# Performance work log

Hardware: AMD Instinct MI355X
Metric: run time of the kernel (lower is better)

Reference implementation:

```python
import jax, jax.numpy as jnp
import numpy as np

K = 16
EPS = 1e-5
NEG_SLOPE = 0.2


def leaky(x):
    return jnp.where(x > 0, x, NEG_SLOPE * x)


def batchnorm_train(x, gamma, beta):
    # x: [B, D]; training-mode BN with biased variance (torch semantics)
    mean = jnp.mean(x, axis=0)
    var = jnp.mean((x - mean) ** 2, axis=0)
    return (x - mean) * jax.lax.rsqrt(var + EPS) * gamma + beta


def setup_inputs() -> dict:
    key = jax.random.key(0)
    ks = jax.random.split(key, 20)
    N, M, D = 30000, 8000, 16
    s = lambda fan_in: 1.0 / np.sqrt(fan_in)
    inp = {
        "xyz": jax.random.normal(ks[0], (N, 3), jnp.float32),
        "atom_xyz": jax.random.normal(ks[1], (M, 3), jnp.float32),
        "atom_types": jax.random.normal(ks[2], (M, D), jnp.float32),
        "Wt1": jax.random.uniform(ks[3], (D, D), jnp.float32, -s(D), s(D)),
        "bt1": jax.random.uniform(ks[4], (D,), jnp.float32, -s(D), s(D)),
        "Wt2": jax.random.uniform(ks[5], (D, D), jnp.float32, -s(D), s(D)),
        "bt2": jax.random.uniform(ks[6], (D,), jnp.float32, -s(D), s(D)),
        "Wt3": jax.random.uniform(ks[7], (D, D), jnp.float32, -s(D), s(D)),
        "bt3": jax.random.uniform(ks[8], (D,), jnp.float32, -s(D), s(D)),
        # embed: conv1 Linear(D+1, D), conv2 Linear(D, D), conv3 Linear(2D, D)
        "W1": jax.random.uniform(ks[9], (D + 1, D), jnp.float32, -s(D + 1), s(D + 1)),
        "b1": jax.random.uniform(ks[10], (D,), jnp.float32, -s(D + 1), s(D + 1)),
        "W2": jax.random.uniform(ks[11], (D, D), jnp.float32, -s(D), s(D)),
        "b2": jax.random.uniform(ks[12], (D,), jnp.float32, -s(D), s(D)),
        "W3": jax.random.uniform(ks[13], (2 * D, D), jnp.float32, -s(2 * D), s(2 * D)),
        "b3": jax.random.uniform(ks[14], (D,), jnp.float32, -s(2 * D), s(2 * D)),
        # batchnorm affine params
        "g1": jnp.ones((D,), jnp.float32),
        "be1": jnp.zeros((D,), jnp.float32),
        "g2": jnp.ones((D,), jnp.float32),
        "be2": jnp.zeros((D,), jnp.float32),
    }
    return inp


def reference(xyz, atom_xyz, atom_types,
              Wt1, bt1, Wt2, bt2, Wt3, bt3,
              W1, b1, W2, b2, W3, b3, g1, be1, g2, be2):
    N, D = xyz.shape[0], atom_types.shape[1]

    # transform_types MLP on atom features: [M, D]
    t = leaky(atom_types @ Wt1 + bt1)
    t = leaky(t @ Wt2 + bt2)
    t = leaky(t @ Wt3 + bt3)

    # kNN: squared distances via GEMM expansion (avoids [N,M,3])
    d2 = (jnp.sum(xyz ** 2, axis=1, keepdims=True)
          + jnp.sum(atom_xyz ** 2, axis=1)[None, :]
          - 2.0 * xyz @ atom_xyz.T)                      # [N, M]
    _, idx = jax.lax.top_k(-d2, K)                       # [N, K] nearest atoms

    # gather neighbor coords, recompute exact squared dists (as in source)
    y_ik = atom_xyz[idx]                                 # [N, K, 3]
    dists = jnp.sum((xyz[:, None, :] - y_ik) ** 2, axis=-1)  # [N, K]

    feat = jnp.concatenate([t[idx], (1.0 / dists)[..., None]], axis=-1)  # [N,K,D+1]

    # conv1 -> leaky -> bn1 -> sum-pool
    fx = feat @ W1 + b1                                  # [N, K, D]
    fx = batchnorm_train(leaky(fx).reshape(-1, D), g1, be1).reshape(N, K, D)
    fx1 = fx.sum(axis=1)                                 # [N, D]

    # conv2 -> leaky -> bn2 -> sum-pool
    fx = fx @ W2 + b2
    fx = batchnorm_train(leaky(fx).reshape(-1, D), g2, be2).reshape(N, K, D)
    fx2 = fx.sum(axis=1)                                 # [N, D]

    return jnp.concatenate([fx1, fx2], axis=-1) @ W3 + b3  # [N, D]
```

## Files before the change

### kernel.cpp

```cpp
#include <hip/hip_runtime.h>

#define N_PTS   30000
#define M_ATOMS 8000
#define D       16
#define KNN     16
#define NGRP    125
#define EPS     1e-5f
#define SLOPE   0.2f
#define BN_COUNT 480000.0f

typedef unsigned long long ull;

__device__ __forceinline__ float leaky(float x) { return x > 0.f ? x : SLOPE * x; }

__device__ __forceinline__ unsigned fkey(float f) {
  unsigned u = __float_as_uint(f);
  return u ^ ((u & 0x80000000u) ? 0xFFFFFFFFu : 0x80000000u);
}
__device__ __forceinline__ float unfkey(unsigned e) {
  unsigned u = (e & 0x80000000u) ? (e ^ 0x80000000u) : ~e;
  return __uint_as_float(u);
}

#define DPPSTEP32(v, CTRL) {                                                   \
  unsigned t_ = (unsigned)__builtin_amdgcn_update_dpp(-1, (int)(v), CTRL, 0xF, 0xF, false); \
  (v) = t_ < (v) ? t_ : (v); }

__device__ __forceinline__ unsigned wmin32d(unsigned v) {
  DPPSTEP32(v, 0x111); DPPSTEP32(v, 0x112); DPPSTEP32(v, 0x114);
  DPPSTEP32(v, 0x118); DPPSTEP32(v, 0x142); DPPSTEP32(v, 0x143);
  return (unsigned)__builtin_amdgcn_readlane((int)v, 63);
}

__device__ __forceinline__ void cswap(ull& a, ull& b) {
  ull mn = a < b ? a : b, mx = a < b ? b : a;
  a = mn; b = mx;
}

__device__ __forceinline__ int morton_cell(float x, float y, float z) {
  int cx = min(max((int)floorf((x + 4.f) * 2.f), 0), 15);
  int cy = min(max((int)floorf((y + 4.f) * 2.f), 0), 15);
  int cz = min(max((int)floorf((z + 4.f) * 2.f), 0), 15);
  int c = 0;
#pragma unroll
  for (int b = 0; b < 4; ++b)
    c |= (((cx>>b)&1) << (3*b)) | (((cy>>b)&1) << (3*b+1)) | (((cz>>b)&1) << (3*b+2));
  return c;
}

__global__ void __launch_bounds__(1024) kB_hist_scan(
    const float* __restrict__ atom_xyz, int* __restrict__ cursors,
    float* __restrict__ gstats, unsigned* __restrict__ benc) {
  __shared__ int h0[4096], h1[4096];
  int tid = threadIdx.x;
  for (int i = tid; i < 4096; i += 1024) h0[i] = 0;
  if (tid < 288) gstats[tid] = 0.f;
  if (tid >= 288 && tid < 663) benc[tid - 288] = 0xFFFFFFFFu;
  if (tid >= 663 && tid < 1024) benc[tid - 288] = 0u;
  if (tid < 14) benc[736 + tid] = 0u;
  __syncthreads();
  for (int m = tid; m < M_ATOMS; m += 1024) {
    int c = morton_cell(atom_xyz[m*3], atom_xyz[m*3+1], atom_xyz[m*3+2]);
    atomicAdd(&h0[c], 1);
  }
  __syncthreads();
  int* src = h0; int* dst = h1;
  for (int off = 1; off < 4096; off <<= 1) {
    for (int i = tid; i < 4096; i += 1024) {
      int v = src[i];
      if (i >= off) v += src[i-off];
      dst[i] = v;
    }
    __syncthreads();
    int* t = src; src = dst; dst = t;
  }
  for (int i = tid; i < 4096; i += 1024) cursors[i] = i ? src[i-1] : 0;
}

#define LAYER(IN, OUT, W, B)                                        \
  _Pragma("unroll") for (int j = 0; j < 16; ++j) {                  \
    float acc = B[j];                                               \
    _Pragma("unroll") for (int i = 0; i < 16; ++i)                  \
      acc = fmaf(IN[i], W[i*16+j], acc);                            \
    OUT[j] = leaky(acc);                                            \
  }

__global__ void __launch_bounds__(256) kC_scatter_mlp(
    const float* __restrict__ atom_xyz, const float* __restrict__ atom_types,
    const float* __restrict__ Wt1, const float* __restrict__ bt1,
    const float* __restrict__ Wt2, const float* __restrict__ bt2,
    const float* __restrict__ Wt3, const float* __restrict__ bt3,
    const float* __restrict__ W1, const float* __restrict__ b1,
    int* __restrict__ cursors, float4* __restrict__ atoms4s,
    int* __restrict__ origid, unsigned* __restrict__ benc,
    float* __restrict__ tu_out) {
  __shared__ float w1[256], w2[256], w3[256], wc[256];
  __shared__ float bb1[16], bb2[16], bb3[16], bbc[16];
  int tid = threadIdx.x;
  w1[tid] = Wt1[tid]; w2[tid] = Wt2[tid]; w3[tid] = Wt3[tid]; wc[tid] = W1[tid];
  if (tid < 16) { bb1[tid] = bt1[tid]; bb2[tid] = bt2[tid];
                  bb3[tid] = bt3[tid]; bbc[tid] = b1[tid]; }
  __syncthreads();
  int m = blockIdx.x * 256 + tid;
  if (m >= M_ATOMS) return;

  float x = atom_xyz[m*3], y = atom_xyz[m*3+1], z = atom_xyz[m*3+2];
  int c = morton_cell(x, y, z);
  int pos = atomicAdd(&cursors[c], 1);
  atoms4s[pos] = make_float4(x, y, z, fmaf(x,x, fmaf(y,y, z*z)));
  origid[pos] = m;
  int g = pos >> 6;
  atomicMin(&benc[g],       fkey(x)); atomicMax(&benc[375+g], fkey(x));
  atomicMin(&benc[125+g],   fkey(y)); atomicMax(&benc[500+g], fkey(y));
  atomicMin(&benc[250+g],   fkey(z)); atomicMax(&benc[625+g], fkey(z));

  float u[16], v[16];
  const float4* tp = (const float4*)(atom_types + (size_t)m*16);
  float4 q0 = tp[0], q1 = tp[1], q2 = tp[2], q3 = tp[3];
  u[0]=q0.x; u[1]=q0.y; u[2]=q0.z; u[3]=q0.w;
  u[4]=q1.x; u[5]=q1.y; u[6]=q1.z; u[7]=q1.w;
  u[8]=q2.x; u[9]=q2.y; u[10]=q2.z; u[11]=q2.w;
  u[12]=q3.x; u[13]=q3.y; u[14]=q3.z; u[15]=q3.w;
  LAYER(u, v, w1, bb1);
  LAYER(v, u, w2, bb2);
  LAYER(u, v, w3, bb3);
  float up[16];
#pragma unroll
  for (int j = 0; j < 16; ++j) {
    float acc = bbc[j];
#pragma unroll
    for (int i = 0; i < 16; ++i) acc = fmaf(v[i], wc[i*16+j], acc);
    up[j] = acc;
  }
  float4* op = (float4*)(tu_out + (size_t)m*16);
  op[0] = make_float4(up[0], up[1], up[2], up[3]);
  op[1] = make_float4(up[4], up[5], up[6], up[7]);
  op[2] = make_float4(up[8], up[9], up[10], up[11]);
  op[3] = make_float4(up[12], up[13], up[14], up[15]);
}

__global__ void __launch_bounds__(256) k2_knn(
    const float* __restrict__ xyz, const float4* __restrict__ atoms4s,
    const int* __restrict__ origid, const unsigned* __restrict__ benc,
    const float* __restrict__ atom_xyz, const float* __restrict__ tu,
    const float* __restrict__ W1,
    int2* __restrict__ pairs, float* __restrict__ gstats) {
  __shared__ float sbuf[4*16*20];
  int tid = threadIdx.x;
  int lane = tid & 63;
  int wid = tid >> 6;
  int n = blockIdx.x * 4 + wid;

  float px = xyz[n*3+0], py = xyz[n*3+1], pz = xyz[n*3+2];
  float x2 = fmaf(px,px, fmaf(py,py, pz*pz));

  unsigned ea, eb = 0xFFFFFFFFu;
  {
    int g = lane;
    float mnx = unfkey(benc[g]),     mny = unfkey(benc[125+g]), mnz = unfkey(benc[250+g]);
    float mxx = unfkey(benc[375+g]), mxy = unfkey(benc[500+g]), mxz = unfkey(benc[625+g]);
    float dx = fmaxf(fmaxf(mnx - px, px - mxx), 0.f);
    float dy = fmaxf(fmaxf(mny - py, py - mxy), 0.f);
    float dz = fmaxf(fmaxf(mnz - pz, pz - mxz), 0.f);
    float lb = fmaf(dx,dx, fmaf(dy,dy, dz*dz)) * 0.999f - 1e-4f;
    ea = (fkey(lb) & 0xFFFFFF00u) | (unsigned)g;
  }
  if (lane + 64 < NGRP) {
    int g = lane + 64;
    float mnx = unfkey(benc[g]),     mny = unfkey(benc[125+g]), mnz = unfkey(benc[250+g]);
    float mxx = unfkey(benc[375+g]), mxy = unfkey(benc[500+g]), mxz = unfkey(benc[625+g]);
    float dx = fmaxf(fmaxf(mnx - px, px - mxx), 0.f);
    float dy = fmaxf(fmaxf(mny - py, py - mxy), 0.f);
    float dz = fmaxf(fmaxf(mnz - pz, pz - mxz), 0.f);
    float lb = fmaf(dx,dx, fmaf(dy,dy, dz*dz)) * 0.999f - 1e-4f;
    eb = (fkey(lb) & 0xFFFFFF00u) | (unsigned)g;
  }
  unsigned cur = ea < eb ? ea : eb;
  unsigned bak = ea < eb ? eb : ea;

  int gs[4];
#pragma unroll
  for (int r = 0; r < 4; ++r) {
    unsigned m = wmin32d(cur);
    bool own = (cur == m);
    cur = own ? bak : cur;
    bak = own ? 0xFFFFFFFFu : bak;
    gs[r] = (int)(m & 0xFFu);
  }

  float4 A[4]; int OI[4];
#pragma unroll
  for (int r = 0; r < 4; ++r) {
    int base = gs[r] << 6;
    A[r]  = atoms4s[base + lane];
    OI[r] = origid [base + lane];
  }
  ull E[4];
#pragma unroll
  for (int r = 0; r < 4; ++r) {
    float dotp = fmaf(px,A[r].x, fmaf(py,A[r].y, pz*A[r].z));
    float d2 = (x2 + A[r].w) - 2.f*dotp;
    E[r] = ((ull)fkey(d2) << 32) | (unsigned)OI[r];
  }
  cswap(E[0],E[1]); cswap(E[2],E[3]); cswap(E[0],E[2]);
  cswap(E[1],E[3]); cswap(E[1],E[2]);
  unsigned cf0 = (unsigned)(E[0] >> 32), ci0 = (unsigned)E[0];
  unsigned cf1 = (unsigned)(E[1] >> 32), ci1 = (unsigned)E[1];
  unsigned cf2 = (unsigned)(E[2] >> 32), ci2 = (unsigned)E[2];
  unsigned cf3 = (unsigned)(E[3] >> 32), ci3 = (unsigned)E[3];

  ull res = ~0ull;
  unsigned mf = 0, mi = 0;
  for (int r = 0; r < KNN; ++r) {
    mf = wmin32d(cf0);
    ull ball = __ballot(cf0 == mf);
    if (__popcll(ball) == 1) {
      int srcl = (int)(__ffsll(ball) - 1);
      mi = (unsigned)__builtin_amdgcn_readlane((int)ci0, srcl);
    } else {
      unsigned cand = (cf0 == mf) ? ci0 : 0xFFFFFFFFu;
      mi = wmin32d(cand);
    }
    bool own = (cf0 == mf) && (ci0 == mi);
    if (lane == r) res = (((ull)mf) << 32) | mi;
    cf0 = own ? cf1 : cf0; cf1 = own ? cf2 : cf1;
    cf2 = own ? cf3 : cf2; cf3 = own ? 0xFFFFFFFFu : cf3;
    ci0 = own ? ci1 : ci0; ci1 = own ? ci2 : ci1;
    ci2 = own ? ci3 : ci2; ci3 = own ? 0xFFFFFFFFu : ci3;
  }
  ull lv = res;
  ull thresh = (((ull)mf) << 32) | mi;

  for (int it = 0; it < NGRP - 4; ++it) {
    unsigned m = wmin32d(cur);
    if ((m & 0xFFFFFF00u) >= (unsigned)(thresh >> 32)) break;
    bool own = (cur == m);
    cur = own ? bak : cur;
    bak = own ? 0xFFFFFFFFu : bak;
    int base = (int)(m & 0xFFu) << 6;

    float4 a = atoms4s[base + lane];
    int oi2 = origid[base + lane];
    float dotp = fmaf(px,a.x, fmaf(py,a.y, pz*a.z));
    float d2 = (x2 + a.w) - 2.f*dotp;
    ull key = ((ull)fkey(d2) << 32) | (unsigned)oi2;

    ull mk = __ballot(key < thresh);
    while (mk) {
      int src = (int)(__ffsll(mk) - 1);
      mk &= mk - 1;
      unsigned klo = (unsigned)__builtin_amdgcn_readlane((int)(unsigned)key, src);
      unsigned khi = (unsigned)__builtin_amdgcn_readlane((int)(unsigned)(key >> 32), src);
      ull kc = ((ull)khi << 32) | klo;
      if (kc < thresh) {
        bool ins = (lane < KNN) && (kc < lv);
        unsigned pvlo = (unsigned)__builtin_amdgcn_update_dpp(0, (int)(unsigned)lv,        0x111, 0xF, 0xF, false);
        unsigned pvhi = (unsigned)__builtin_amdgcn_update_dpp(0, (int)(unsigned)(lv>>32), 0x111, 0xF, 0xF, false);
        int pins      =           __builtin_amdgcn_update_dpp(0, ins ? 1 : 0,              0x111, 0xF, 0xF, false);
        if (ins) lv = pins ? (((ull)pvhi << 32) | pvlo) : kc;
        unsigned tlo = (unsigned)__builtin_amdgcn_readlane((int)(unsigned)lv, KNN-1);
        unsigned thi = (unsigned)__builtin_amdgcn_readlane((int)(unsigned)(lv >> 32), KNN-1);
        thresh = ((ull)thi << 32) | tlo;
      }
    }
  }

  int oi = (int)(unsigned)(lv & 0xFFFFFFFFull);
  float iv = 0.f;
  if (lane < KNN) {
    float bx = atom_xyz[oi*3+0], by = atom_xyz[oi*3+1], bz = atom_xyz[oi*3+2];
    float dx = px - bx, dy = py - by, dz = pz - bz;
    float dd = fmaf(dx,dx, fmaf(dy,dy, dz*dz));
    iv = 1.f / dd;
    pairs[n*KNN + lane] = make_int2(oi, __float_as_int(iv));

    const float4* up4 = (const float4*)(tu + (size_t)oi*16);
    float4 u0 = up4[0], u1 = up4[1], u2 = up4[2], u3 = up4[3];
    float4* row = (float4*)&sbuf[(wid*16 + lane)*20];
    float4 w;
    w.x = leaky(fmaf(iv, W1[256+ 0], u0.x)); w.y = leaky(fmaf(iv, W1[256+ 1], u0.y));
    w.z = leaky(fmaf(iv, W1[256+ 2], u0.z)); w.w = leaky(fmaf(iv, W1[256+ 3], u0.w));
    row[0] = w;
    w.x = leaky(fmaf(iv, W1[256+ 4], u1.x)); w.y = leaky(fmaf(iv, W1[256+ 5], u1.y));
    w.z = leaky(fmaf(iv, W1[256+ 6], u1.z)); w.w = leaky(fmaf(iv, W1[256+ 7], u1.w));
    row[1] = w;
    w.x = leaky(fmaf(iv, W1[256+ 8], u2.x)); w.y = leaky(fmaf(iv, W1[256+ 9], u2.y));
    w.z = leaky(fmaf(iv, W1[256+10], u2.z)); w.w = leaky(fmaf(iv, W1[256+11], u2.w));
    row[2] = w;
    w.x = leaky(fmaf(iv, W1[256+12], u3.x)); w.y = leaky(fmaf(iv, W1[256+13], u3.y));
    w.z = leaky(fmaf(iv, W1[256+14], u3.z)); w.w = leaky(fmaf(iv, W1[256+15], u3.w));
    row[3] = w;
  }
  __syncthreads();
  {
    int ch = tid & 15, grp = tid >> 4;
    float S = 0.f, Q = 0.f;
#pragma unroll
    for (int i = 0; i < 4; ++i) {
      float v = sbuf[(grp*4 + i)*20 + ch];
      S += v; Q += v*v;
    }
    __syncthreads();
    sbuf[grp*20 + ch] = S;
    sbuf[400 + grp*20 + ch] = Q;
  }
  __syncthreads();
  if (tid < 32) {
    int ch = tid & 15;
    int off = (tid < 16) ? 0 : 400;
    float s = 0.f;
#pragma unroll
    for (int g = 0; g < 16; ++g) s += sbuf[off + g*20 + ch];
    atomicAdd(&gstats[(blockIdx.x & 7)*32 + tid], s);
  }
}

__device__ __forceinline__ void a1_row(const float* __restrict__ tu, int idx,
                                       float iv, const float* wiv, float* a) {
  const float4* up = (const float4*)(tu + (size_t)idx*16);
  float4 r0 = up[0], r1 = up[1], r2 = up[2], r3 = up[3];
  float u[16];
  u[0]=r0.x; u[1]=r0.y; u[2]=r0.z; u[3]=r0.w;
  u[4]=r1.x; u[5]=r1.y; u[6]=r1.z; u[7]=r1.w;
  u[8]=r2.x; u[9]=r2.y; u[10]=r2.z; u[11]=r2.w;
  u[12]=r3.x; u[13]=r3.y; u[14]=r3.z; u[15]=r3.w;
#pragma unroll
  for (int j = 0; j < 16; ++j) a[j] = leaky(fmaf(iv, wiv[j], u[j]));
}

__global__ void __launch_bounds__(256, 4) k4_main(
    const int2* __restrict__ pairs, const float* __restrict__ tu,
    const float* __restrict__ W1,
    const float* __restrict__ W2, const float* __restrict__ b2,
    const float* __restrict__ g1, const float* __restrict__ be1,
    float* __restrict__ fx1_out, float* __restrict__ s2_out,
    float* __restrict__ gstats) {
  __shared__ float wiv[16], w2s[256], b2s[16];
  __shared__ float sc1[16], sh1[16];
  __shared__ float buf[16*16*17];
  int tid = threadIdx.x;
  w2s[tid] = W2[tid];
  if (tid < 16) { wiv[tid] = W1[256 + tid]; b2s[tid] = b2[tid]; }
  if (tid < 16) {
    float s1 = 0.f, q1 = 0.f;
#pragma unroll
    for (int c = 0; c < 8; ++c) { s1 += gstats[c*32 + tid]; q1 += gstats[c*32 + 16 + tid]; }
    float mean = s1 * (1.f/BN_COUNT);
    float var  = q1 * (1.f/BN_COUNT) - mean*mean;
    float sC = g1[tid] / sqrtf(var + EPS);
    sc1[tid] = sC;
    sh1[tid] = be1[tid] - mean * sC;
  }
  __syncthreads();

  int g = blockIdx.x * 256 + tid;
  int p = tid >> 4, k = tid & 15;
  int2 pr = pairs[g];
  int idx = pr.x;
  float iv = __int_as_float(pr.y);
  float h[16], a2[16];
  a1_row(tu, idx, iv, wiv, h);
#pragma unroll
  for (int j = 0; j < 16; ++j) h[j] = fmaf(h[j], sc1[j], sh1[j]);
#pragma unroll
  for (int j = 0; j < 16; ++j) {
    float accj = b2s[j];
#pragma unroll
    for (int i = 0; i < 16; ++i) accj = fmaf(h[i], w2s[i*16+j], accj);
    a2[j] = leaky(accj);
  }

  float* myrow = &buf[(p*16 + k)*17];
  int p2 = tid >> 4, j2 = tid & 15;
#pragma unroll
  for (int j = 0; j < 16; ++j) myrow[j] = h[j];
  __syncthreads();
  {
    float s = 0.f;
#pragma unroll
    for (int kk = 0; kk < 16; ++kk) s += buf[(p2*16+kk)*17 + j2];
    fx1_out[(size_t)blockIdx.x*256 + tid] = s;
  }
  __syncthreads();
#pragma unroll
  for (int j = 0; j < 16; ++j) myrow[j] = a2[j];
  __syncthreads();
  float s2v = 0.f;
#pragma unroll
  for (int kk = 0; kk < 16; ++kk) s2v += buf[(p2*16+kk)*17 + j2];
  s2_out[(size_t)blockIdx.x*256 + tid] = s2v;
  __syncthreads();
#pragma unroll
  for (int j = 0; j < 16; ++j) myrow[j] = a2[j]*a2[j];
  __syncthreads();
  float q2v = 0.f;
#pragma unroll
  for (int kk = 0; kk < 16; ++kk) q2v += buf[(p2*16+kk)*17 + j2];
  __syncthreads();
  buf[p2*17 + j2] = s2v;
  buf[289 + p2*17 + j2] = q2v;
  __syncthreads();
  if (tid < 16) {
    float t1 = 0.f, t2 = 0.f;
#pragma unroll
    for (int pp = 0; pp < 16; ++pp) { t1 += buf[pp*17 + tid]; t2 += buf[289 + pp*17 + tid]; }
    atomicAdd(&gstats[256 + tid], t1);
    atomicAdd(&gstats[272 + tid], t2);
  }
}

__global__ void __launch_bounds__(256) k5_final(
    const float* __restrict__ fx1_in, const float* __restrict__ s2_in,
    const float* __restrict__ gstats,
    const float* __restrict__ W3, const float* __restrict__ b3,
    const float* __restrict__ g2, const float* __restrict__ be2,
    float* __restrict__ out) {
  __shared__ float w[512], bb[16], sc2[16], sh2[16];
  int tid = threadIdx.x;
  w[tid] = W3[tid]; w[256+tid] = W3[256+tid];
  if (tid < 16) {
    bb[tid] = b3[tid];
    float mean = gstats[256+tid] * (1.f/BN_COUNT);
    float var  = gstats[272+tid] * (1.f/BN_COUNT) - mean*mean;
    float s = g2[tid] / sqrtf(var + EPS);
    sc2[tid] = s;
    sh2[tid] = be2[tid] - mean * s;
  }
  __syncthreads();
  int n = blockIdx.x * 256 + tid;
  if (n >= N_PTS) return;

  const float4* f1p = (const float4*)(fx1_in + (size_t)n*16);
  const float4* f2p = (const float4*)(s2_in  + (size_t)n*16);
  float4 x0=f1p[0], x1=f1p[1], x2=f1p[2], x3=f1p[3];
  float4 y0=f2p[0], y1=f2p[1], y2=f2p[2], y3=f2p[3];
  float f1[16] = {x0.x,x0.y,x0.z,x0.w, x1.x,x1.y,x1.z,x1.w,
                  x2.x,x2.y,x2.z,x2.w, x3.x,x3.y,x3.z,x3.w};
  float f2[16] = {y0.x,y0.y,y0.z,y0.w, y1.x,y1.y,y1.z,y1.w,
                  y2.x,y2.y,y2.z,y2.w, y3.x,y3.y,y3.z,y3.w};
#pragma unroll
  for (int i = 0; i < 16; ++i) f2[i] = fmaf(sc2[i], f2[i], 16.f * sh2[i]);

  float4* op = (float4*)(out + (size_t)n*16);
  float o[16];
#pragma unroll
  for (int j = 0; j < 16; ++j) {
    float accj = bb[j];
#pragma unroll
    for (int i = 0; i < 16; ++i) accj = fmaf(f1[i], w[i*16+j], accj);
#pragma unroll
    for (int i = 0; i < 16; ++i) accj = fmaf(f2[i], w[(16+i)*16+j], accj);
    o[j] = accj;
  }
  op[0] = make_float4(o[0], o[1], o[2], o[3]);
  op[1] = make_float4(o[4], o[5], o[6], o[7]);
  op[2] = make_float4(o[8], o[9], o[10], o[11]);
  op[3] = make_float4(o[12], o[13], o[14], o[15]);
}

extern "C" void kernel_launch(void* const* d_in, const int* in_sizes, int n_in,
                              void* d_out, int out_size, void* d_ws, size_t ws_size,
                              hipStream_t stream) {
  const float* xyz        = (const float*)d_in[0];
  const float* atom_xyz   = (const float*)d_in[1];
  const float* atom_types = (const float*)d_in[2];
  const float* Wt1 = (const float*)d_in[3];  const float* bt1 = (const float*)d_in[4];
  const float* Wt2 = (const float*)d_in[5];  const float* bt2 = (const float*)d_in[6];
  const float* Wt3 = (const float*)d_in[7];  const float* bt3 = (const float*)d_in[8];
  const float* W1  = (const float*)d_in[9];  const float* b1  = (const float*)d_in[10];
  const float* W2  = (const float*)d_in[11]; const float* b2  = (const float*)d_in[12];
  const float* W3  = (const float*)d_in[13]; const float* b3  = (const float*)d_in[14];
  const float* g1  = (const float*)d_in[15]; const float* be1 = (const float*)d_in[16];
  const float* g2  = (const float*)d_in[17]; const float* be2 = (const float*)d_in[18];
  float* out = (float*)d_out;

  float* ws = (float*)d_ws;
  float*    tu      = ws;
  int2*     pairs   = (int2*)(ws + 128000);
  float*    fx1     = ws + 1088000;
  float*    s2      = ws + 1568000;
  float*    gstats  = ws + 2048000;
  int*      cursors = (int*)(ws + 2048288);
  unsigned* benc    = (unsigned*)(ws + 2052384);
  float4*   atoms4s = (float4*)(ws + 1088000);
  int*      origid  = (int*)(ws + 1120000);

  kB_hist_scan<<<1, 1024, 0, stream>>>(atom_xyz, cursors, gstats, benc);
  kC_scatter_mlp<<<32, 256, 0, stream>>>(atom_xyz, atom_types, Wt1, bt1,
                                         Wt2, bt2, Wt3, bt3, W1, b1,
                                         cursors, atoms4s, origid, benc, tu);
  k2_knn<<<7500, 256, 0, stream>>>(xyz, atoms4s, origid, benc, atom_xyz,
                                   tu, W1, pairs, gstats);
  k4_main<<<1875, 256, 0, stream>>>(pairs, tu, W1, W2, b2, g1, be1,
                                    fx1, s2, gstats);
  k5_final<<<118, 256, 0, stream>>>(fx1, s2, gstats, W3, b3, g2, be2, out);
}
```

Baseline: 215.5 us.

## Replace sorted kNN seeding with radix-select threshold and unsorted candidate set

The initial top-16 is now chosen by a bitwise radix select over the 256 candidate keys using ballot/popcount, instead of 16 rounds of wavefront min extraction. Survivors are compacted through shared memory into an unsorted 16-lane list. During later insertion, the current maximum is replaced and a DPP 64-bit max reduction recomputes the threshold, instead of shifting a sorted list. This removes serial min-extraction rounds, but each radix select costs 32 iterations of 4 ballots, and each insertion now pays a full 64-bit max reduction.

```diff
diff --git a/kernel.cpp b/kernel.cpp
--- a/kernel.cpp
+++ b/kernel.cpp
@@ -32,9 +32,20 @@
   return (unsigned)__builtin_amdgcn_readlane((int)v, 63);
 }
 
-__device__ __forceinline__ void cswap(ull& a, ull& b) {
-  ull mn = a < b ? a : b, mx = a < b ? b : a;
-  a = mn; b = mx;
+#define DPPSTEP64MAX(lo, hi, CTRL) {                                           \
+  unsigned tlo_ = (unsigned)__builtin_amdgcn_update_dpp(0, (int)(lo), CTRL, 0xF, 0xF, false); \
+  unsigned thi_ = (unsigned)__builtin_amdgcn_update_dpp(0, (int)(hi), CTRL, 0xF, 0xF, false); \
+  bool gt_ = (thi_ > (hi)) || ((thi_ == (hi)) && (tlo_ > (lo)));               \
+  (lo) = gt_ ? tlo_ : (lo); (hi) = gt_ ? thi_ : (hi); }
+
+__device__ __forceinline__ ull wmax64d(ull v) {
+  unsigned lo = (unsigned)v, hi = (unsigned)(v >> 32);
+  DPPSTEP64MAX(lo, hi, 0x111); DPPSTEP64MAX(lo, hi, 0x112);
+  DPPSTEP64MAX(lo, hi, 0x114); DPPSTEP64MAX(lo, hi, 0x118);
+  DPPSTEP64MAX(lo, hi, 0x142); DPPSTEP64MAX(lo, hi, 0x143);
+  unsigned flo = (unsigned)__builtin_amdgcn_readlane((int)lo, 63);
+  unsigned fhi = (unsigned)__builtin_amdgcn_readlane((int)hi, 63);
+  return ((ull)fhi << 32) | flo;
 }
 
 __device__ __forceinline__ int morton_cell(float x, float y, float z) {
@@ -145,7 +156,7 @@
     const float* __restrict__ atom_xyz, const float* __restrict__ tu,
     const float* __restrict__ W1,
     int2* __restrict__ pairs, float* __restrict__ gstats) {
-  __shared__ float sbuf[4*16*20];
+  __shared__ float sbuf[4*16*20 + 128];
   int tid = threadIdx.x;
   int lane = tid & 63;
   int wid = tid >> 6;
@@ -195,41 +206,69 @@
     A[r]  = atoms4s[base + lane];
     OI[r] = origid [base + lane];
   }
-  ull E[4];
-#pragma unroll
-  for (int r = 0; r < 4; ++r) {
-    float dotp = fmaf(px,A[r].x, fmaf(py,A[r].y, pz*A[r].z));
-    float d2 = (x2 + A[r].w) - 2.f*dotp;
-    E[r] = ((ull)fkey(d2) << 32) | (unsigned)OI[r];
-  }
-  cswap(E[0],E[1]); cswap(E[2],E[3]); cswap(E[0],E[2]);
-  cswap(E[1],E[3]); cswap(E[1],E[2]);
-  unsigned cf0 = (unsigned)(E[0] >> 32), ci0 = (unsigned)E[0];
-  unsigned cf1 = (unsigned)(E[1] >> 32), ci1 = (unsigned)E[1];
-  unsigned cf2 = (unsigned)(E[2] >> 32), ci2 = (unsigned)E[2];
-  unsigned cf3 = (unsigned)(E[3] >> 32), ci3 = (unsigned)E[3];
-
-  ull res = ~0ull;
-  unsigned mf = 0, mi = 0;
-  for (int r = 0; r < KNN; ++r) {
-    mf = wmin32d(cf0);
-    ull ball = __ballot(cf0 == mf);
-    if (__popcll(ball) == 1) {
-      int srcl = (int)(__ffsll(ball) - 1);
-      mi = (unsigned)__builtin_amdgcn_readlane((int)ci0, srcl);
-    } else {
-      unsigned cand = (cf0 == mf) ? ci0 : 0xFFFFFFFFu;
-      mi = wmin32d(cand);
+  unsigned cf0, cf1, cf2, cf3, ci0, ci1, ci2, ci3;
+  {
+    float d0 = (x2 + A[0].w) - 2.f*fmaf(px,A[0].x, fmaf(py,A[0].y, pz*A[0].z));
+    float d1 = (x2 + A[1].w) - 2.f*fmaf(px,A[1].x, fmaf(py,A[1].y, pz*A[1].z));
+    float d2 = (x2 + A[2].w) - 2.f*fmaf(px,A[2].x, fmaf(py,A[2].y, pz*A[2].z));
+    float d3 = (x2 + A[3].w) - 2.f*fmaf(px,A[3].x, fmaf(py,A[3].y, pz*A[3].z));
+    cf0 = fkey(d0); cf1 = fkey(d1); cf2 = fkey(d2); cf3 = fkey(d3);
+    ci0 = (unsigned)OI[0]; ci1 = (unsigned)OI[1];
+    ci2 = (unsigned)OI[2]; ci3 = (unsigned)OI[3];
+  }
+
+  unsigned F = 0;
+  for (int b = 31; b >= 0; --b) {
+    unsigned x = F | (1u << b);
+    int c = __popcll(__ballot(cf0 < x)) + __popcll(__ballot(cf1 < x))
+          + __popcll(__ballot(cf2 < x)) + __popcll(__ballot(cf3 < x));
+    if (c < KNN) F = x;
+  }
+  ull m0 = __ballot(cf0 == F), m1 = __ballot(cf1 == F);
+  ull m2 = __ballot(cf2 == F), m3 = __ballot(cf3 == F);
+  int c_eq = __popcll(m0) + __popcll(m1) + __popcll(m2) + __popcll(m3);
+  unsigned I;
+  if (c_eq == 1) {
+    if (m0)      I = (unsigned)__builtin_amdgcn_readlane((int)ci0, (int)(__ffsll(m0)-1));
+    else if (m1) I = (unsigned)__builtin_amdgcn_readlane((int)ci1, (int)(__ffsll(m1)-1));
+    else if (m2) I = (unsigned)__builtin_amdgcn_readlane((int)ci2, (int)(__ffsll(m2)-1));
+    else         I = (unsigned)__builtin_amdgcn_readlane((int)ci3, (int)(__ffsll(m3)-1));
+  } else {
+    int c_lt = __popcll(__ballot(cf0 < F)) + __popcll(__ballot(cf1 < F))
+             + __popcll(__ballot(cf2 < F)) + __popcll(__ballot(cf3 < F));
+    int j = KNN - c_lt;
+    unsigned P = 0;
+    for (int b = 31; b >= 0; --b) {
+      unsigned x = P | (1u << b);
+      int c = __popcll(__ballot(cf0 == F && ci0 < x))
+            + __popcll(__ballot(cf1 == F && ci1 < x))
+            + __popcll(__ballot(cf2 == F && ci2 < x))
+            + __popcll(__ballot(cf3 == F && ci3 < x));
+      if (c < j) P = x;
     }
-    bool own = (cf0 == mf) && (ci0 == mi);
-    if (lane == r) res = (((ull)mf) << 32) | mi;
-    cf0 = own ? cf1 : cf0; cf1 = own ? cf2 : cf1;
-    cf2 = own ? cf3 : cf2; cf3 = own ? 0xFFFFFFFFu : cf3;
-    ci0 = own ? ci1 : ci0; ci1 = own ? ci2 : ci1;
-    ci2 = own ? ci3 : ci2; ci3 = own ? 0xFFFFFFFFu : ci3;
-  }
-  ull lv = res;
-  ull thresh = (((ull)mf) << 32) | mi;
+    I = P;
+  }
+  ull T = ((ull)F << 32) | I;
+
+  {
+    unsigned* scr = (unsigned*)&sbuf[4*16*20 + wid*32];
+    ull E0 = ((ull)cf0 << 32) | ci0, E1 = ((ull)cf1 << 32) | ci1;
+    ull E2 = ((ull)cf2 << 32) | ci2, E3 = ((ull)cf3 << 32) | ci3;
+    bool s0 = E0 <= T, s1 = E1 <= T, s2 = E2 <= T, s3 = E3 <= T;
+    ull b0 = __ballot(s0), b1 = __ballot(s1), b2 = __ballot(s2), b3 = __ballot(s3);
+    ull below = (lane == 63) ? 0x7FFFFFFFFFFFFFFFull : ((1ull << lane) - 1ull);
+    int n0 = __popcll(b0), n1 = __popcll(b1), n2 = __popcll(b2);
+    if (s0) { int p = __popcll(b0 & below);           scr[p] = cf0; scr[16+p] = ci0; }
+    if (s1) { int p = n0 + __popcll(b1 & below);      scr[p] = cf1; scr[16+p] = ci1; }
+    if (s2) { int p = n0+n1 + __popcll(b2 & below);   scr[p] = cf2; scr[16+p] = ci2; }
+    if (s3) { int p = n0+n1+n2 + __popcll(b3 & below);scr[p] = cf3; scr[16+p] = ci3; }
+  }
+  ull lv = 0;
+  {
+    unsigned* scr = (unsigned*)&sbuf[4*16*20 + wid*32];
+    if (lane < KNN) lv = ((ull)scr[lane] << 32) | scr[16+lane];
+  }
+  ull thresh = T;
 
   for (int it = 0; it < NGRP - 4; ++it) {
     unsigned m = wmin32d(cur);
@@ -253,14 +292,10 @@
       unsigned khi = (unsigned)__builtin_amdgcn_readlane((int)(unsigned)(key >> 32), src);
       ull kc = ((ull)khi << 32) | klo;
       if (kc < thresh) {
-        bool ins = (lane < KNN) && (kc < lv);
-        unsigned pvlo = (unsigned)__builtin_amdgcn_update_dpp(0, (int)(unsigned)lv,        0x111, 0xF, 0xF, false);
-        unsigned pvhi = (unsigned)__builtin_amdgcn_update_dpp(0, (int)(unsigned)(lv>>32), 0x111, 0xF, 0xF, false);
-        int pins      =           __builtin_amdgcn_update_dpp(0, ins ? 1 : 0,              0x111, 0xF, 0xF, false);
-        if (ins) lv = pins ? (((ull)pvhi << 32) | pvlo) : kc;
-        unsigned tlo = (unsigned)__builtin_amdgcn_readlane((int)(unsigned)lv, KNN-1);
-        unsigned thi = (unsigned)__builtin_amdgcn_readlane((int)(unsigned)(lv >> 32), KNN-1);
-        thresh = ((ull)thi << 32) | tlo;
+        ull ball2 = __ballot(lv == thresh);
+        int vl = (int)(__ffsll(ball2) - 1);
+        if (lane == vl) lv = kc;
+        thresh = wmax64d(lv);
       }
     }
   }
```

After: 236.6 us. 1.1x slower.
